# Performance work log

Measured on AMD Instinct MI355X. Metric: run time of the kernel, lower is better.

The kernel has to match this reference:

```python
import jax, jax.numpy as jnp
import numpy as np

EPS = 1e-8  # matches torch F.cosine_similarity eps

def _unit(x):
    return x / jnp.maximum(jnp.linalg.norm(x, axis=-1, keepdims=True), EPS)

def setup_inputs() -> dict:
    key = jax.random.key(0)
    k1, = jax.random.split(key, 1)
    S, U, D = 512, 32, 1024
    embeddings = jax.random.normal(k1, (S * U, D), dtype=jnp.float32)
    return {
        "embeddings": embeddings,
        "w": jnp.float32(10.0),
        "b": jnp.float32(-5.0),
        "num_speakers": S,
        "utterances_per_speaker": U,
    }

def reference(embeddings, w, b, num_speakers, utterances_per_speaker):
    S, U = num_speakers, utterances_per_speaker
    emb = embeddings.reshape(S, U, -1)                      # (S,U,D)
    csum = emb.sum(axis=1)                                  # (S,D)
    cent_incl = csum / U                                    # inclusive centroids
    cent_excl = (csum[:, None, :] - emb) / (U - 1)          # (S,U,D) leave-one-out

    e = _unit(emb)
    ci = _unit(cent_incl)
    ce = _unit(cent_excl)

    # cosine similarity of every utterance vs every inclusive centroid
    sim = jnp.einsum('sud,kd->suk', e, ci)                  # (S,U,S)
    # replace own-speaker column with exclusive-centroid similarity
    diag = jnp.sum(e * ce, axis=-1)                         # (S,U)
    idx = jnp.arange(S)
    sim = sim.at[idx, :, idx].set(diag)

    logits = w * sim + b                                    # (S,U,S)
    logp = jax.nn.log_softmax(logits, axis=-1)
    # cross-entropy with target = own speaker, averaged over all S*U utterances
    loss = -jnp.mean(logp[idx, :, idx])
    return loss
```

## Files before the change

kernel.cpp:

```cpp
#include <hip/hip_runtime.h>
#include <hip/hip_bf16.h>
#include <math.h>

#define S_ 512
#define U_ 32
#define D_ 1024
#define M_ (S_ * U_)

typedef __attribute__((ext_vector_type(8))) short bf16x8;
typedef __attribute__((ext_vector_type(4))) float f32x4;

__device__ __forceinline__ unsigned int f2bf(float f) {
    union { float f; unsigned u; } v; v.f = f;
    return (v.u + 0x7FFFu + ((v.u >> 16) & 1u)) >> 16;
}
__device__ __forceinline__ bf16x8 cvt8(float4 u, float4 v) {
    union { bf16x8 b; unsigned r[4]; } o;
    asm("v_cvt_pk_bf16_f32 %0, %1, %2" : "=v"(o.r[0]) : "v"(u.x), "v"(u.y));
    asm("v_cvt_pk_bf16_f32 %0, %1, %2" : "=v"(o.r[1]) : "v"(u.z), "v"(u.w));
    asm("v_cvt_pk_bf16_f32 %0, %1, %2" : "=v"(o.r[2]) : "v"(v.x), "v"(v.y));
    asm("v_cvt_pk_bf16_f32 %0, %1, %2" : "=v"(o.r[3]) : "v"(v.z), "v"(v.w));
    return o.b;
}


__global__ __launch_bounds__(256) void ge2e_prep_t(
    const float* __restrict__ emb, unsigned short* __restrict__ ebf_t,
    unsigned short* __restrict__ cib_t, float* __restrict__ rn2,
    float* __restrict__ csn)
{
    const int s = blockIdx.x, t = threadIdx.x, w = t >> 6, l = t & 63;
    __shared__ __align__(16) unsigned short tile[16][1032];
    __shared__ float sqw[16][4];
    __shared__ float red[4];
    __shared__ __align__(16) unsigned short crow[1024];

    const int panel = s >> 2;
    float4 psum = make_float4(0.f, 0.f, 0.f, 0.f);

    #pragma unroll
    for (int P = 0; P < 2; ++P) {
        const float* base = emb + ((size_t)s * 32 + P * 16) * D_ + t * 4;
        float q[16];
        #pragma unroll
        for (int u = 0; u < 16; ++u) {
            float4 v = *(const float4*)(base + (size_t)u * D_);
            psum.x += v.x; psum.y += v.y; psum.z += v.z; psum.w += v.w;
            q[u] = v.x * v.x + v.y * v.y + v.z * v.z + v.w * v.w;
            ushort4 o;
            o.x = (unsigned short)f2bf(v.x); o.y = (unsigned short)f2bf(v.y);
            o.z = (unsigned short)f2bf(v.z); o.w = (unsigned short)f2bf(v.w);
            *(ushort4*)&tile[u][t * 4] = o;
        }
        #pragma unroll
        for (int u = 0; u < 16; ++u) {
            float qq = q[u];
            #pragma unroll
            for (int m = 1; m < 64; m <<= 1) qq += __shfl_xor(qq, m);
            if (l == 0) sqw[u][w] = qq;
        }
        __syncthreads();
        if (t < 16) rn2[s * 32 + P * 16 + t] = sqw[t][0] + sqw[t][1] + sqw[t][2] + sqw[t][3];
        const int fi = (s & 3) * 2 + P;
        #pragma unroll
        for (int it = 0; it < 8; ++it) {
            const int unit = it * 256 + t;
            const int kc = unit >> 6, g = (unit >> 4) & 3, r15 = unit & 15;
            uint4 d = *(const uint4*)&tile[r15][kc * 32 + g * 8];
            const size_t gu = (((size_t)(panel * 32 + kc)) * 8 + fi) * 64 + g * 16 + r15;
            *(uint4*)(ebf_t + gu * 8) = d;
        }
        __syncthreads();
    }

    float cn = psum.x * psum.x + psum.y * psum.y + psum.z * psum.z + psum.w * psum.w;
    #pragma unroll
    for (int m = 1; m < 64; m <<= 1) cn += __shfl_xor(cn, m);
    if (l == 0) red[w] = cn;
    __syncthreads();
    const float csn2 = red[0] + red[1] + red[2] + red[3];
    const float inv = rsqrtf(csn2);
    if (t == 0) csn[s] = sqrtf(csn2);
    {
        ushort4 o;
        o.x = (unsigned short)f2bf(psum.x * inv); o.y = (unsigned short)f2bf(psum.y * inv);
        o.z = (unsigned short)f2bf(psum.z * inv); o.w = (unsigned short)f2bf(psum.w * inv);
        *(ushort4*)&crow[t * 4] = o;
    }
    __syncthreads();
    if (t < 128) {
        const int kc = t >> 2, gg = t & 3;
        const int cp = s >> 7, nf = (s & 127) >> 4, c15 = s & 15;
        uint4 d = *(const uint4*)&crow[t * 8];
        const size_t gu = (((size_t)(cp * 32 + kc)) * 8 + nf) * 64 + gg * 16 + c15;
        *(uint4*)(cib_t + gu * 8) = d;
    }
}

__global__ __launch_bounds__(256, 3) void ge2e_gemm_t(
    const unsigned short* __restrict__ ebf_t, const unsigned short* __restrict__ cib_t,
    const float* __restrict__ rn2, const float* __restrict__ csn,
    const float* __restrict__ wp, const float* __restrict__ bp,
    float* __restrict__ rowsum, float* __restrict__ tgt)
{
    __shared__ __align__(16) short sA[2][4096];
    __shared__ __align__(16) short sB[2][4096];
    __shared__ float sRn2[128];
    __shared__ float sPart[128][2];

    const int t = threadIdx.x, w = t >> 6, l = t & 63;
    const int wm = w >> 1, wn = w & 1, g = l >> 4, c = l & 15;
    const int bid = blockIdx.x, brow = bid >> 2, bcol = bid & 3;

    const unsigned short* At = ebf_t + (size_t)(brow * 32) * 4096;
    const unsigned short* Bt = cib_t + (size_t)(bcol * 32) * 4096;

    if (t < 128) sRn2[t] = rn2[brow * 128 + t];

    f32x4 acc[4][4];
    #pragma unroll
    for (int i = 0; i < 4; ++i)
        #pragma unroll
        for (int j = 0; j < 4; ++j) acc[i][j] = (f32x4){0.f, 0.f, 0.f, 0.f};

    uint4 ra0, ra1, rb0, rb1;
#define LOADREG(kc) { const unsigned short* a_ = At + (kc) * 4096; \
                      const unsigned short* b_ = Bt + (kc) * 4096; \
                      ra0 = *(const uint4*)(a_ + t * 8);        \
                      ra1 = *(const uint4*)(a_ + 2048 + t * 8); \
                      rb0 = *(const uint4*)(b_ + t * 8);        \
                      rb1 = *(const uint4*)(b_ + 2048 + t * 8); }
#define WRITELDS(buf) { *(uint4*)&sA[buf][t * 8] = ra0; *(uint4*)&sA[buf][2048 + t * 8] = ra1; \
                        *(uint4*)&sB[buf][t * 8] = rb0; *(uint4*)&sB[buf][2048 + t * 8] = rb1; }

    LOADREG(0); WRITELDS(0);
    __syncthreads();

    for (int kc = 0; kc < 32; ++kc) {
        const int cb = kc & 1;
        if (kc < 31) LOADREG(kc + 1);
        bf16x8 af[4], bb[4];
        #pragma unroll
        for (int i = 0; i < 4; ++i) {
            af[i] = *(const bf16x8*)&sA[cb][((wm * 4 + i) * 64 + l) * 8];
            bb[i] = *(const bf16x8*)&sB[cb][((wn * 4 + i) * 64 + l) * 8];
        }
        __builtin_amdgcn_s_setprio(1);
        #pragma unroll
        for (int i = 0; i < 4; ++i)
            #pragma unroll
            for (int j = 0; j < 4; ++j)
                acc[i][j] = __builtin_amdgcn_mfma_f32_16x16x32_bf16(af[i], bb[j], acc[i][j], 0, 0, 0);
        __builtin_amdgcn_s_setprio(0);
        if (kc < 31) WRITELDS(cb ^ 1);
        __syncthreads();
    }
#undef LOADREG
#undef WRITELDS

    const float W = wp[0], Bb = bp[0];
    const float Cs = Bb + fabsf(W);
    #pragma unroll
    for (int mi = 0; mi < 4; ++mi) {
        #pragma unroll
        for (int r = 0; r < 4; ++r) {
            const int row_local = wm * 64 + mi * 16 + g * 4 + r;
            const int gr = brow * 128 + row_local;
            const int sid = gr >> 5;
            const float rn2v = sRn2[row_local];
            const float invr = rsqrtf(rn2v);
            float se = 0.f;
            #pragma unroll
            for (int ni = 0; ni < 4; ++ni) {
                const int col = bcol * 128 + wn * 64 + ni * 16 + c;
                const float a = acc[mi][ni][r];
                float sim = a * invr;
                if (col == sid) {
                    const float csnv = csn[sid];
                    const float dotv = a * csnv;
                    const float ex2 = fmaxf(csnv * csnv - 2.f * dotv + rn2v, 1e-12f);
                    sim = (dotv - rn2v) * invr * rsqrtf(ex2);
                }
                const float lg = fmaf(W, sim, Bb);
                if (col == sid) tgt[gr] = lg;
                se += expf(lg - Cs);
            }
            #pragma unroll
            for (int m = 1; m < 16; m <<= 1) se += __shfl_xor(se, m);
            if (c == 0) sPart[row_local][wn] = se;
        }
    }
    __syncthreads();
    if (t < 128) atomicAdd(&rowsum[brow * 128 + t], sPart[t][0] + sPart[t][1]);
}

__global__ __launch_bounds__(256) void ge2e_lse(
    const float* __restrict__ rowsum, const float* __restrict__ tgt,
    const float* __restrict__ wp, const float* __restrict__ bp,
    float* __restrict__ lossAcc)
{
    __shared__ float red[4];
    const int t = threadIdx.x, gr = blockIdx.x * 256 + t;
    const float Cs = bp[0] + fabsf(wp[0]);
    float contrib = logf(rowsum[gr]) + Cs - tgt[gr];
    #pragma unroll
    for (int m = 1; m < 64; m <<= 1) contrib += __shfl_xor(contrib, m);
    if ((t & 63) == 0) red[t >> 6] = contrib;
    __syncthreads();
    if (t == 0) atomicAdd(lossAcc, red[0] + red[1] + red[2] + red[3]);
}

__global__ void ge2e_final(const float* __restrict__ lossAcc, float* __restrict__ out)
{
    out[0] = lossAcc[0] * (1.0f / (float)M_);
}

__global__ __launch_bounds__(256) void ge2e_prep_fb(
    const float* __restrict__ emb, unsigned short* __restrict__ cib,
    float* __restrict__ rn2, float* __restrict__ csn)
{
    const int s = blockIdx.x, t = threadIdx.x, w = t >> 6, l = t & 63;
    __shared__ float scs[4][1024];
    __shared__ float red[4];
    float cs[16];
    #pragma unroll
    for (int i = 0; i < 16; ++i) cs[i] = 0.f;
    for (int uu = 0; uu < 8; ++uu) {
        const int u = w * 8 + uu;
        const size_t roff = ((size_t)s * U_ + u) * D_ + l * 16;
        const float4* rp = (const float4*)(emb + roff);
        const float4 v0 = rp[0], v1 = rp[1], v2 = rp[2], v3 = rp[3];
        cs[0] += v0.x; cs[1] += v0.y; cs[2] += v0.z; cs[3] += v0.w;
        cs[4] += v1.x; cs[5] += v1.y; cs[6] += v1.z; cs[7] += v1.w;
        cs[8] += v2.x; cs[9] += v2.y; cs[10] += v2.z; cs[11] += v2.w;
        cs[12] += v3.x; cs[13] += v3.y; cs[14] += v3.z; cs[15] += v3.w;
        float q = v0.x*v0.x + v0.y*v0.y + v0.z*v0.z + v0.w*v0.w
                + v1.x*v1.x + v1.y*v1.y + v1.z*v1.z + v1.w*v1.w
                + v2.x*v2.x + v2.y*v2.y + v2.z*v2.z + v2.w*v2.w
                + v3.x*v3.x + v3.y*v3.y + v3.z*v3.z + v3.w*v3.w;
        #pragma unroll
        for (int m = 1; m < 64; m <<= 1) q += __shfl_xor(q, m);
        if (l == 0) rn2[s * U_ + u] = q;
    }
    #pragma unroll
    for (int i = 0; i < 16; ++i) scs[w][l * 16 + i] = cs[i];
    __syncthreads();
    float4 p0 = *(const float4*)&scs[0][t * 4], p1 = *(const float4*)&scs[1][t * 4];
    float4 p2 = *(const float4*)&scs[2][t * 4], p3 = *(const float4*)&scs[3][t * 4];
    float4 tot; tot.x = p0.x+p1.x+p2.x+p3.x; tot.y = p0.y+p1.y+p2.y+p3.y;
    tot.z = p0.z+p1.z+p2.z+p3.z; tot.w = p0.w+p1.w+p2.w+p3.w;
    float cn = tot.x*tot.x + tot.y*tot.y + tot.z*tot.z + tot.w*tot.w;
    #pragma unroll
    for (int m = 1; m < 64; m <<= 1) cn += __shfl_xor(cn, m);
    if (l == 0) red[w] = cn;
    __syncthreads();
    const float csn2 = red[0] + red[1] + red[2] + red[3];
    const float inv = rsqrtf(csn2);
    if (t == 0) csn[s] = sqrtf(csn2);
    ushort4 o;
    o.x = (unsigned short)f2bf(tot.x * inv); o.y = (unsigned short)f2bf(tot.y * inv);
    o.z = (unsigned short)f2bf(tot.z * inv); o.w = (unsigned short)f2bf(tot.w * inv);
    *(ushort4*)(cib + (size_t)s * D_ + t * 4) = o;
}

__global__ __launch_bounds__(512, 4) void ge2e_fused_fb(
    const float* __restrict__ emb, const unsigned short* __restrict__ cib,
    const float* __restrict__ rn2, const float* __restrict__ csn,
    const float* __restrict__ wp, const float* __restrict__ bp,
    float* __restrict__ lossAcc)
{
    __shared__ float sMax[32][8], sSum[32][8], sTgt[32];
    const int t = threadIdx.x, row0 = blockIdx.x * 32;
    const int w = t >> 6, l = t & 63, g = l >> 4, c = l & 15;
    const float* aF0 = emb + (size_t)(row0 + c) * D_ + g * 8;
    const float* aF1 = aF0 + (size_t)16 * D_;
    const unsigned short* bB = cib + (size_t)(w * 64 + c) * D_ + g * 8;
    f32x4 acc[2][4];
    #pragma unroll
    for (int m = 0; m < 2; ++m)
        #pragma unroll
        for (int n = 0; n < 4; ++n) acc[m][n] = (f32x4){0.f, 0.f, 0.f, 0.f};
    bf16x8 as[3][2], bs[3][4];
#define LOADK(slot, kk) do { \
        const float4* p0 = (const float4*)(aF0 + (kk) * 32); \
        const float4* p1 = (const float4*)(aF1 + (kk) * 32); \
        as[slot][0] = cvt8(p0[0], p0[1]); as[slot][1] = cvt8(p1[0], p1[1]); \
        bs[slot][0] = *(const bf16x8*)(bB + (kk) * 32); \
        bs[slot][1] = *(const bf16x8*)(bB + (size_t)16 * D_ + (kk) * 32); \
        bs[slot][2] = *(const bf16x8*)(bB + (size_t)32 * D_ + (kk) * 32); \
        bs[slot][3] = *(const bf16x8*)(bB + (size_t)48 * D_ + (kk) * 32); } while (0)
    LOADK(0, 0); LOADK(1, 1);
    #pragma unroll
    for (int ks = 0; ks < 32; ++ks) {
        if (ks + 2 < 32) LOADK((ks + 2) % 3, ks + 2);
        const int cu = ks % 3;
        #pragma unroll
        for (int n = 0; n < 4; ++n) {
            acc[0][n] = __builtin_amdgcn_mfma_f32_16x16x32_bf16(as[cu][0], bs[cu][n], acc[0][n], 0, 0, 0);
            acc[1][n] = __builtin_amdgcn_mfma_f32_16x16x32_bf16(as[cu][1], bs[cu][n], acc[1][n], 0, 0, 0);
        }
    }
#undef LOADK
    const float W = wp[0], Bb = bp[0];
    const int s = blockIdx.x, wsid = s >> 6, jn = (s >> 4) & 3, cdiag = s & 15;
    const float csnv = csn[s];
    const bool dlane = (w == wsid) && (c == cdiag);
    #pragma unroll
    for (int m = 0; m < 2; ++m) {
        #pragma unroll
        for (int r = 0; r < 4; ++r) {
            const int lr = m * 16 + g * 4 + r;
            const float rn2v = rn2[row0 + lr];
            const float invr = rsqrtf(rn2v);
            float vals[4], mx = -1e30f, tg = 0.f;
            #pragma unroll
            for (int n = 0; n < 4; ++n) {
                const float a = acc[m][n][r];
                float sim = a * invr;
                if (dlane && n == jn) {
                    const float dotv = a * csnv;
                    const float ex2 = fmaxf(csnv * csnv - 2.f * dotv + rn2v, 1e-12f);
                    sim = (dotv - rn2v) * invr * rsqrtf(ex2);
                }
                const float lg = fmaf(W, sim, Bb);
                vals[n] = lg;
                if (dlane && n == jn) tg = lg;
                mx = fmaxf(mx, lg);
            }
            #pragma unroll
            for (int msk = 1; msk < 16; msk <<= 1) mx = fmaxf(mx, __shfl_xor(mx, msk));
            float se = 0.f;
            #pragma unroll
            for (int n = 0; n < 4; ++n) se += expf(vals[n] - mx);
            #pragma unroll
            for (int msk = 1; msk < 16; msk <<= 1) se += __shfl_xor(se, msk);
            if (c == 0) { sMax[lr][w] = mx; sSum[lr][w] = se; }
            if (dlane) sTgt[lr] = tg;
        }
    }
    __syncthreads();
    if (t < 32) {
        float Mx = -1e30f;
        #pragma unroll
        for (int q = 0; q < 8; ++q) Mx = fmaxf(Mx, sMax[t][q]);
        float Ss = 0.f;
        #pragma unroll
        for (int q = 0; q < 8; ++q) Ss += sSum[t][q] * expf(sMax[t][q] - Mx);
        float contrib = Mx + logf(Ss) - sTgt[t];
        #pragma unroll
        for (int msk = 1; msk < 32; msk <<= 1) contrib += __shfl_xor(contrib, msk);
        if (t == 0) atomicAdd(lossAcc, contrib);
    }
}

extern "C" void kernel_launch(void* const* d_in, const int* in_sizes, int n_in,
                              void* d_out, int out_size, void* d_ws, size_t ws_size,
                              hipStream_t stream)
{
    const float* emb = (const float*)d_in[0];
    const float* wp  = (const float*)d_in[1];
    const float* bp  = (const float*)d_in[2];

    float* ws = (float*)d_ws;
    float* rn2     = ws;
    float* csn     = ws + 16384;
    float* rowsum  = ws + 16896;
    float* tgt     = ws + 33280;
    float* lossAcc = ws + 49664;
    unsigned short* cib_t = (unsigned short*)(ws + 49668);
    unsigned short* ebf_t = cib_t + (size_t)S_ * D_;

    const size_t need = (size_t)49668 * 4 + (size_t)S_ * D_ * 2 + (size_t)M_ * D_ * 2;

    hipMemsetAsync(lossAcc, 0, sizeof(float), stream);

    if (ws_size >= need) {
        hipMemsetAsync(rowsum, 0, M_ * sizeof(float), stream);
        ge2e_prep_t<<<S_, 256, 0, stream>>>(emb, ebf_t, cib_t, rn2, csn);
        ge2e_gemm_t<<<(M_ / 128) * 4, 256, 0, stream>>>(ebf_t, cib_t, rn2, csn, wp, bp, rowsum, tgt);
        ge2e_lse<<<M_ / 256, 256, 0, stream>>>(rowsum, tgt, wp, bp, lossAcc);
    } else {
        unsigned short* cib = (unsigned short*)(ws + 16900);
        ge2e_prep_fb<<<S_, 256, 0, stream>>>(emb, cib, rn2, csn);
        ge2e_fused_fb<<<M_ / 32, 512, 0, stream>>>(emb, cib, rn2, csn, wp, bp, lossAcc);
    }
    ge2e_final<<<1, 1, 0, stream>>>(lossAcc, (float*)d_out);
}
```

Before: 146.1 us.

## Stage GEMM tiles via direct global-to-LDS loads and swizzle block order

```diff
diff --git a/kernel.cpp b/kernel.cpp
--- a/kernel.cpp
+++ b/kernel.cpp
@@ -21,6 +21,12 @@
     asm("v_cvt_pk_bf16_f32 %0, %1, %2" : "=v"(o.r[2]) : "v"(v.x), "v"(v.y));
     asm("v_cvt_pk_bf16_f32 %0, %1, %2" : "=v"(o.r[3]) : "v"(v.z), "v"(v.w));
     return o.b;
+}
+
+__device__ __forceinline__ void gl16(const void* g, void* l) {
+    __builtin_amdgcn_global_load_lds(
+        (__attribute__((address_space(1))) void*)(void*)g,
+        (__attribute__((address_space(3))) void*)l, 16, 0, 0);
 }
 
 
@@ -110,7 +116,8 @@
 
     const int t = threadIdx.x, w = t >> 6, l = t & 63;
     const int wm = w >> 1, wn = w & 1, g = l >> 4, c = l & 15;
-    const int bid = blockIdx.x, brow = bid >> 2, bcol = bid & 3;
+    const int logical = (blockIdx.x & 7) * 64 + (blockIdx.x >> 3);
+    const int brow = logical >> 2, bcol = logical & 3;
 
     const unsigned short* At = ebf_t + (size_t)(brow * 32) * 4096;
     const unsigned short* Bt = cib_t + (size_t)(bcol * 32) * 4096;
@@ -123,22 +130,21 @@
         #pragma unroll
         for (int j = 0; j < 4; ++j) acc[i][j] = (f32x4){0.f, 0.f, 0.f, 0.f};
 
-    uint4 ra0, ra1, rb0, rb1;
-#define LOADREG(kc) { const unsigned short* a_ = At + (kc) * 4096; \
-                      const unsigned short* b_ = Bt + (kc) * 4096; \
-                      ra0 = *(const uint4*)(a_ + t * 8);        \
-                      ra1 = *(const uint4*)(a_ + 2048 + t * 8); \
-                      rb0 = *(const uint4*)(b_ + t * 8);        \
-                      rb1 = *(const uint4*)(b_ + 2048 + t * 8); }
-#define WRITELDS(buf) { *(uint4*)&sA[buf][t * 8] = ra0; *(uint4*)&sA[buf][2048 + t * 8] = ra1; \
-                        *(uint4*)&sB[buf][t * 8] = rb0; *(uint4*)&sB[buf][2048 + t * 8] = rb1; }
-
-    LOADREG(0); WRITELDS(0);
+#define STAGE(kcn, buf) { \
+        const unsigned short* a_ = At + (size_t)(kcn) * 4096; \
+        const unsigned short* b_ = Bt + (size_t)(kcn) * 4096; \
+        gl16(a_ + ((w * 2 + 0) * 64 + l) * 8, &sA[buf][(w * 2 + 0) * 512]); \
+        gl16(a_ + ((w * 2 + 1) * 64 + l) * 8, &sA[buf][(w * 2 + 1) * 512]); \
+        gl16(b_ + ((w * 2 + 0) * 64 + l) * 8, &sB[buf][(w * 2 + 0) * 512]); \
+        gl16(b_ + ((w * 2 + 1) * 64 + l) * 8, &sB[buf][(w * 2 + 1) * 512]); \
+    }
+
+    STAGE(0, 0);
     __syncthreads();
 
     for (int kc = 0; kc < 32; ++kc) {
         const int cb = kc & 1;
-        if (kc < 31) LOADREG(kc + 1);
+        if (kc < 31) STAGE(kc + 1, cb ^ 1);
         bf16x8 af[4], bb[4];
         #pragma unroll
         for (int i = 0; i < 4; ++i) {
@@ -152,11 +158,9 @@
             for (int j = 0; j < 4; ++j)
                 acc[i][j] = __builtin_amdgcn_mfma_f32_16x16x32_bf16(af[i], bb[j], acc[i][j], 0, 0, 0);
         __builtin_amdgcn_s_setprio(0);
-        if (kc < 31) WRITELDS(cb ^ 1);
         __syncthreads();
     }
-#undef LOADREG
-#undef WRITELDS
+#undef STAGE
 
     const float W = wp[0], Bb = bp[0];
     const float Cs = Bb + fabsf(W);
```

Result: no change. 148.9 us (+1.9%).
